# Optimization experiments

Hardware: AMD Instinct MI355X
Metric: run time of the kernel (lower is better)

## Reference

```python
import jax, jax.numpy as jnp
import numpy as np

DIM = 1028


def setup_inputs() -> dict:
    key = jax.random.key(0)
    ks = jax.random.split(key, 11)
    B, N = 8, 2048
    s = 0.02
    x = jax.random.normal(ks[0], (B, N, DIM), dtype=jnp.float32)
    Wq = jax.random.normal(ks[1], (DIM, DIM), dtype=jnp.float32) * s
    bq = jax.random.normal(ks[2], (DIM,), dtype=jnp.float32) * s
    Wk = jax.random.normal(ks[3], (DIM, DIM), dtype=jnp.float32) * s
    bk = jax.random.normal(ks[4], (DIM,), dtype=jnp.float32) * s
    Wv = jax.random.normal(ks[5], (DIM, DIM), dtype=jnp.float32) * s
    bv = jax.random.normal(ks[6], (DIM,), dtype=jnp.float32) * s
    We = jax.random.normal(ks[7], (4 * DIM, DIM), dtype=jnp.float32) * s
    be = jax.random.normal(ks[8], (4 * DIM,), dtype=jnp.float32) * s
    Wo = jax.random.normal(ks[9], (DIM, 4 * DIM), dtype=jnp.float32) * s
    bo = jax.random.normal(ks[10], (DIM,), dtype=jnp.float32) * s
    return {"x": x, "Wq": Wq, "bq": bq, "Wk": Wk, "bk": bk, "Wv": Wv,
            "bv": bv, "We": We, "be": be, "Wo": Wo, "bo": bo}


def reference(x, Wq, bq, Wk, bk, Wv, bv, We, be, Wo, bo):
    # x: [B, N, D]. torch Linear weight is [out, in] -> x @ W.T + b
    q = jnp.einsum('bnd,ed->bne', x, Wq) + bq
    k = jnp.einsum('bnd,ed->bne', x, Wk) + bk
    v = jnp.einsum('bnd,ed->bne', x, Wv) + bv
    scores = jnp.einsum('bqd,bkd->bqk', q, k) / jnp.sqrt(jnp.float32(DIM))
    w = jax.nn.softmax(scores, axis=-1)          # [B, N, N]
    attn = jnp.einsum('bqk,bkd->bqd', w, v)      # [B, N, D]
    h = jax.nn.gelu(jnp.einsum('bnd,hd->bnh', attn, We) + be, approximate=False)
    out = jnp.einsum('bnh,dh->bnd', h, Wo) + bo
    return out + x
```

## Files before the change

### kernel.cpp

```cpp
#include <hip/hip_runtime.h>
#include <hip/hip_bf16.h>
#include <cstdint>
#include <cmath>


typedef __bf16 bf16;
typedef __bf16 bf16x8 __attribute__((ext_vector_type(8)));
typedef float  f32x4  __attribute__((ext_vector_type(4)));

#define D_REAL   1028
#define D_PADK   1088
#define D_PADN   1152
#define H_REAL   4112
#define H_PAD    4224
#define NTOK     2048
#define NB       8
#define MTOT     (NB*NTOK)
#define SLAB_X   ((size_t)NTOK*D_PADK)
#define SLAB_S   ((size_t)NTOK*NTOK)
#define WSLAB    ((size_t)D_PADN*D_PADK)
#define VSLAB    ((size_t)D_PADN*NTOK)

__device__ __forceinline__ void async16(const void* g, void* l) {
    __builtin_amdgcn_global_load_lds(
        (__attribute__((address_space(1))) void*)(uintptr_t)g,
        (__attribute__((address_space(3))) void*)(uint32_t)(uintptr_t)l,
        16, 0, 0);
}

#define MFMA_(a, b, c) __builtin_amdgcn_mfma_f32_16x16x32_bf16(a, b, c, 0, 0, 0)

template <int EPI, bool XPIN>
__global__ __launch_bounds__(512, 2)
void gemm256(const bf16* __restrict__ A, size_t strideA,
             const bf16* __restrict__ B, size_t strideB,
             const float* __restrict__ bias, size_t strideBias,
             void* __restrict__ Out, size_t strideOut,
             bf16* __restrict__ OutV,
             int K, int outPitch, int colBound, float scale,
             const float* __restrict__ resid)
{
    __shared__ __attribute__((aligned(16))) bf16 sAB[4][256 * 64];

    int bx, by, bz;
    if (XPIN) {
        bz = blockIdx.x; by = blockIdx.y; bx = blockIdx.z;
    } else {
        const int nx   = gridDim.x;
        const int nwg  = nx * gridDim.y;
        const int orig = blockIdx.y * nx + blockIdx.x;
        const int q    = nwg >> 3;
        const int wg   = (orig & 7) * q + (orig >> 3);
        bx = wg % nx; by = wg / nx; bz = blockIdx.z;
    }

    A += (size_t)bz * strideA;
    B += (size_t)bz * strideB;
    if (bias) bias += (size_t)bz * strideBias;

    const int tid  = threadIdx.x;
    const int lane = tid & 63;
    const int wv   = tid >> 6;
    const int wm   = wv >> 2;
    const int wn   = wv & 3;

    const int    NT  = K >> 6;
    const size_t K64 = (size_t)K * 64;

    const int sRow = tid >> 3;
    const int sCh  = (tid & 7) ^ (sRow & 7);
    const bf16* gA = A + (size_t)(by * 256 + sRow) * K + sCh * 8;
    const bf16* gB = B + (size_t)(bx * 256 + sRow) * K + sCh * 8;
    const int ldsOff = sRow * 64 + (tid & 7) * 8;

#define STAGE_A(tt) do {                                           \
        const bf16* g_ = gA + (size_t)(tt) * 64;                   \
        bf16* l_ = &sAB[(tt) & 1][0] + ldsOff;                     \
        async16(g_,           l_);                                 \
        async16(g_ +     K64, l_ +  4096);                         \
        async16(g_ + 2 * K64, l_ +  8192);                         \
        async16(g_ + 3 * K64, l_ + 12288);                         \
    } while (0)
#define STAGE_B(tt) do {                                           \
        const bf16* g_ = gB + (size_t)(tt) * 64;                   \
        bf16* l_ = &sAB[2 + ((tt) & 1)][0] + ldsOff;               \
        async16(g_,           l_);                                 \
        async16(g_ +     K64, l_ +  4096);                         \
        async16(g_ + 2 * K64, l_ +  8192);                         \
        async16(g_ + 3 * K64, l_ + 12288);                         \
    } while (0)

    const int lr   = lane & 15;
    const int lq   = lane >> 4;
    const int rsw  = lr & 7;
    const int aRow = (wm * 128 + lr) * 64;
    const int bRow = (wn * 64  + lr) * 64;
    const int sl0  = (lq ^ rsw) << 3;
    const int sl1  = ((lq + 4) ^ rsw) << 3;

#define LDA_(i, s) (*(const bf16x8*)&sAc[aRow + (i) * 1024 + (s)])
#define LDB_(j, s) (*(const bf16x8*)&sBc[bRow + (j) * 1024 + (s)])

    f32x4 acc[8][4] = {};

    STAGE_A(0); STAGE_B(0);

    for (int t = 0; t < NT; ++t) {
        if (t + 1 < NT) {
            STAGE_A(t + 1);
            STAGE_B(t + 1);
            asm volatile("s_waitcnt vmcnt(8)" ::: "memory");
        } else {
            asm volatile("s_waitcnt vmcnt(0)" ::: "memory");
        }
        __builtin_amdgcn_s_barrier();
        __builtin_amdgcn_sched_barrier(0);

        const bf16* sAc = &sAB[t & 1][0];
        const bf16* sBc = &sAB[2 + (t & 1)][0];

        bf16x8 bfr[4][2];
        bfr[0][0] = LDB_(0, sl0); bfr[0][1] = LDB_(0, sl1);
        bfr[1][0] = LDB_(1, sl0); bfr[1][1] = LDB_(1, sl1);
        bfr[2][0] = LDB_(2, sl0); bfr[2][1] = LDB_(2, sl1);
        bfr[3][0] = LDB_(3, sl0); bfr[3][1] = LDB_(3, sl1);

        #pragma unroll
        for (int i = 0; i < 8; ++i) {
            const bf16x8 a0 = LDA_(i, sl0);
            const bf16x8 a1 = LDA_(i, sl1);
            acc[i][0] = MFMA_(a0, bfr[0][0], acc[i][0]);
            acc[i][1] = MFMA_(a0, bfr[1][0], acc[i][1]);
            acc[i][2] = MFMA_(a0, bfr[2][0], acc[i][2]);
            acc[i][3] = MFMA_(a0, bfr[3][0], acc[i][3]);
            acc[i][0] = MFMA_(a1, bfr[0][1], acc[i][0]);
            acc[i][1] = MFMA_(a1, bfr[1][1], acc[i][1]);
            acc[i][2] = MFMA_(a1, bfr[2][1], acc[i][2]);
            acc[i][3] = MFMA_(a1, bfr[3][1], acc[i][3]);
        }

        asm volatile("s_waitcnt lgkmcnt(0)" ::: "memory");
        __builtin_amdgcn_s_barrier();
        __builtin_amdgcn_sched_barrier(0);
    }

    #pragma unroll
    for (int i = 0; i < 8; ++i) {
        const int rowBase = by * 256 + wm * 128 + i * 16 + lq * 4;
        #pragma unroll
        for (int j = 0; j < 4; ++j) {
            f32x4 v = acc[i][j];
            const int cg = bx * 256 + wn * 64 + j * 16 + lr;
            if (cg >= colBound) continue;
            const float bs = bias ? bias[cg] : 0.0f;
            #pragma unroll
            for (int r = 0; r < 4; ++r) {
                const int mg = rowBase + r;
                const float val = v[r];
                if (EPI == 0) {
                    ((bf16*)Out + (size_t)bz * strideOut)[(size_t)mg * outPitch + cg] =
                        (bf16)(val + bs);
                } else if (EPI == 3) {
                    const float u = val + bs;
                    const float g = 0.5f * u * (1.0f + erff(u * 0.70710678118654752f));
                    ((bf16*)Out)[(size_t)mg * outPitch + cg] = (bf16)g;
                } else if (EPI == 4) {
                    ((float*)Out)[(size_t)mg * outPitch + cg] =
                        val + bs + resid[(size_t)mg * outPitch + cg];
                } else if (EPI == 5) {
                    const int grp = cg / D_PADN;
                    const int c   = cg - grp * D_PADN;
                    const float u = val + bs;
                    if (grp < 2) {
                        if (c < D_PADK)
                            ((bf16*)Out)[(size_t)bz * 2 * SLAB_X + (size_t)grp * SLAB_X +
                                         (size_t)mg * D_PADK + c] = (bf16)u;
                    } else {
                        OutV[(size_t)bz * VSLAB + (size_t)c * NTOK + mg] = (bf16)u;
                    }
                } else {
                    ((bf16*)Out + (size_t)bz * strideOut)[(size_t)mg * outPitch + cg] =
                        (bf16)(val * scale);
                }
            }
        }
    }
#undef STAGE_A
#undef STAGE_B
#undef LDA_
#undef LDB_
}

__global__ __launch_bounds__(256)
void cvt_pad(const float* __restrict__ src, int R, int C,
             bf16* __restrict__ dst, int CP)
{
    const int c = blockIdx.x * 256 + threadIdx.x;
    const int r = blockIdx.y;
    if (c >= CP) return;
    const float v = (r < R && c < C) ? src[(size_t)r * C + c] : 0.0f;
    dst[(size_t)r * CP + c] = (bf16)v;
}

__global__ __launch_bounds__(256)
void pad_bias(const float* __restrict__ src, int n, float* __restrict__ dst, int np)
{
    const int i = blockIdx.x * 256 + threadIdx.x;
    if (i < np) dst[i] = (i < n) ? src[i] : 0.0f;
}

__global__ __launch_bounds__(256)
void softmax_ip(bf16* __restrict__ S)
{
    const int row  = blockIdx.x * 4 + (threadIdx.x >> 6);
    const int lane = threadIdx.x & 63;
    bf16* s = S + (size_t)row * NTOK + lane * 8;

    float v[32];
    #pragma unroll
    for (int j = 0; j < 4; ++j) {
        bf16x8 t = *(const bf16x8*)(s + j * 512);
        #pragma unroll
        for (int e = 0; e < 8; ++e) v[j * 8 + e] = (float)t[e];
    }
    float m = -1e30f;
    #pragma unroll
    for (int i = 0; i < 32; ++i) m = fmaxf(m, v[i]);
    #pragma unroll
    for (int off = 32; off > 0; off >>= 1) m = fmaxf(m, __shfl_xor(m, off, 64));

    float sum = 0.0f;
    #pragma unroll
    for (int i = 0; i < 32; ++i) { v[i] = __expf(v[i] - m); sum += v[i]; }
    #pragma unroll
    for (int off = 32; off > 0; off >>= 1) sum += __shfl_xor(sum, off, 64);
    const float inv = 1.0f / sum;

    #pragma unroll
    for (int j = 0; j < 4; ++j) {
        bf16x8 t;
        #pragma unroll
        for (int e = 0; e < 8; ++e) t[e] = (bf16)(v[j * 8 + e] * inv);
        *(bf16x8*)(s + j * 512) = t;
    }
}

#define OFF_WQKV   0u
#define OFF_WE     7520256u
#define OFF_WO     16711680u
#define OFF_BQKV   26443776u
#define OFF_BE     26457600u
#define OFF_XBF    26474496u
#define OFF_VT     62126080u
#define OFF_SCR    99874816u
#define QS_BYTES   8912896u
#define SS_BYTES   8388608u

extern "C" void kernel_launch(void* const* d_in, const int* in_sizes, int n_in,
                              void* d_out, int out_size, void* d_ws, size_t ws_size,
                              hipStream_t stream)
{
    const float* x  = (const float*)d_in[0];
    const float* Wq = (const float*)d_in[1];
    const float* bq = (const float*)d_in[2];
    const float* Wk = (const float*)d_in[3];
    const float* bk = (const float*)d_in[4];
    const float* Wv = (const float*)d_in[5];
    const float* bv = (const float*)d_in[6];
    const float* We = (const float*)d_in[7];
    const float* be = (const float*)d_in[8];
    const float* Wo = (const float*)d_in[9];
    const float* bo = (const float*)d_in[10];

    char* ws = (char*)d_ws;
    bf16*  Wqkv = (bf16*)(ws + OFF_WQKV);
    bf16*  WeP  = (bf16*)(ws + OFF_WE);
    bf16*  WoP  = (bf16*)(ws + OFF_WO);
    float* Bqkv = (float*)(ws + OFF_BQKV);
    float* BeP  = (float*)(ws + OFF_BE);
    bf16*  Xbf  = (bf16*)(ws + OFF_XBF);
    bf16*  Vt   = (bf16*)(ws + OFF_VT);
    char*  scr  = ws + OFF_SCR;

    const size_t avail = ws_size > OFF_SCR ? ws_size - OFF_SCR : 0;
    const size_t perG  = (size_t)QS_BYTES + SS_BYTES;
    int G = (avail >= 8 * perG) ? 8 : (avail >= 4 * perG) ? 4
          : (avail >= 2 * perG) ? 2 : 1;
    int R = (avail >= 69206016u) ? 8192 : (avail >= 34603008u) ? 4096 : 2048;

    bf16* Qs = (bf16*)scr;
    bf16* Ss = (bf16*)(scr + (size_t)G * QS_BYTES);
    bf16* Hb = (bf16*)scr;

    const dim3 blk(256);
    const dim3 blkG(512);
    const float inv_sqrt_d = (float)(1.0 / sqrt((double)D_REAL));

    cvt_pad<<<dim3(5, MTOT), blk, 0, stream>>>(x, MTOT, D_REAL, Xbf, D_PADK);
    cvt_pad<<<dim3(5, D_PADN), blk, 0, stream>>>(Wq, D_REAL, D_REAL, Wqkv, D_PADK);
    cvt_pad<<<dim3(5, D_PADN), blk, 0, stream>>>(Wk, D_REAL, D_REAL, Wqkv + WSLAB, D_PADK);
    cvt_pad<<<dim3(5, D_PADN), blk, 0, stream>>>(Wv, D_REAL, D_REAL, Wqkv + 2 * WSLAB, D_PADK);
    cvt_pad<<<dim3(5, H_PAD), blk, 0, stream>>>(We, H_REAL, D_REAL, WeP, D_PADK);
    cvt_pad<<<dim3(17, D_PADN), blk, 0, stream>>>(Wo, D_REAL, H_REAL, WoP, H_PAD);
    pad_bias<<<dim3(5), blk, 0, stream>>>(bq, D_REAL, Bqkv, D_PADN);
    pad_bias<<<dim3(5), blk, 0, stream>>>(bk, D_REAL, Bqkv + D_PADN, D_PADN);
    pad_bias<<<dim3(5), blk, 0, stream>>>(bv, D_REAL, Bqkv + 2 * D_PADN, D_PADN);
    pad_bias<<<dim3(17), blk, 0, stream>>>(be, H_REAL, BeP, H_PAD);

    for (int g0 = 0; g0 < NB; g0 += G) {
        gemm256<5, false><<<dim3(14, 8, G), blkG, 0, stream>>>(
            Xbf + (size_t)g0 * SLAB_X, SLAB_X, Wqkv, 0, Bqkv, 0,
            Qs, 0, Vt + (size_t)g0 * VSLAB,
            D_PADK, 0, 3456, 1.0f, nullptr);
        gemm256<6, true><<<dim3(G, 8, 8), blkG, 0, stream>>>(
            Qs, 2 * SLAB_X, Qs + SLAB_X, 2 * SLAB_X, nullptr, 0,
            Ss, SLAB_S, nullptr, D_PADK, NTOK, NTOK, inv_sqrt_d, nullptr);
        softmax_ip<<<dim3(G * 512), blk, 0, stream>>>(Ss);
        gemm256<0, true><<<dim3(G, 8, 5), blkG, 0, stream>>>(
            Ss, SLAB_S, Vt + (size_t)g0 * VSLAB, VSLAB, nullptr, 0,
            Xbf + (size_t)g0 * SLAB_X, SLAB_X, nullptr,
            NTOK, D_PADK, D_PADK, 1.0f, nullptr);
    }

    for (int r0 = 0; r0 < MTOT; r0 += R) {
        gemm256<3, false><<<dim3(17, R / 256, 1), blkG, 0, stream>>>(
            Xbf + (size_t)r0 * D_PADK, 0, WeP, 0, BeP, 0,
            Hb, 0, nullptr, D_PADK, H_PAD, H_PAD, 1.0f, nullptr);
        gemm256<4, false><<<dim3(5, R / 256, 1), blkG, 0, stream>>>(
            Hb, 0, WoP, 0, bo, 0,
            (float*)d_out + (size_t)r0 * D_REAL, 0, nullptr,
            H_PAD, D_REAL, D_REAL, 1.0f, x + (size_t)r0 * D_REAL);
    }
}
```

Baseline: 1.136 ms.

## Interleave split global-to-LDS staging with MFMA phases in GEMM main loop

The bf16 GEMM main loop is split into four compute phases of two row blocks each. The A and B tile loads are broken into halves and issued between these phases: A for the next tile, and B two tiles ahead, since the B fragments are already held in registers. The goal is to overlap global-to-LDS transfers with MFMA work instead of issuing them all at the top of each iteration. The compute sections also raise wave priority with s_setprio. In exchange, the loop needs many more barriers and hand-tuned vmcnt/lgkmcnt waits, and any mistake in that counting risks read-after-write races on the two LDS buffers.

Result: slower. 1.164 ms (+2.5%).

```diff
diff --git a/kernel.cpp b/kernel.cpp
--- a/kernel.cpp
+++ b/kernel.cpp
@@ -73,21 +73,17 @@
     const bf16* gB = B + (size_t)(bx * 256 + sRow) * K + sCh * 8;
     const int ldsOff = sRow * 64 + (tid & 7) * 8;
 
-#define STAGE_A(tt) do {                                           \
-        const bf16* g_ = gA + (size_t)(tt) * 64;                   \
-        bf16* l_ = &sAB[(tt) & 1][0] + ldsOff;                     \
-        async16(g_,           l_);                                 \
-        async16(g_ +     K64, l_ +  4096);                         \
-        async16(g_ + 2 * K64, l_ +  8192);                         \
-        async16(g_ + 3 * K64, l_ + 12288);                         \
+#define STAGE_A_HALF(tt, h) do {                                        \
+        const bf16* g_ = gA + (size_t)(tt) * 64 + (size_t)(2*(h)) * K64;\
+        bf16* l_ = &sAB[(tt) & 1][0] + ldsOff + (2*(h)) * 4096;         \
+        async16(g_,       l_);                                          \
+        async16(g_ + K64, l_ + 4096);                                   \
     } while (0)
-#define STAGE_B(tt) do {                                           \
-        const bf16* g_ = gB + (size_t)(tt) * 64;                   \
-        bf16* l_ = &sAB[2 + ((tt) & 1)][0] + ldsOff;               \
-        async16(g_,           l_);                                 \
-        async16(g_ +     K64, l_ +  4096);                         \
-        async16(g_ + 2 * K64, l_ +  8192);                         \
-        async16(g_ + 3 * K64, l_ + 12288);                         \
+#define STAGE_B_HALF(tt, h) do {                                        \
+        const bf16* g_ = gB + (size_t)(tt) * 64 + (size_t)(2*(h)) * K64;\
+        bf16* l_ = &sAB[2 + ((tt) & 1)][0] + ldsOff + (2*(h)) * 4096;   \
+        async16(g_,       l_);                                          \
+        async16(g_ + K64, l_ + 4096);                                   \
     } while (0)
 
     const int lr   = lane & 15;
@@ -103,45 +99,76 @@
 
     f32x4 acc[8][4] = {};
 
-    STAGE_A(0); STAGE_B(0);
+#define MM(i, x0, x1) do {                                  \
+        acc[i][0] = MFMA_(x0, bfr[0][0], acc[i][0]);        \
+        acc[i][1] = MFMA_(x0, bfr[1][0], acc[i][1]);        \
+        acc[i][2] = MFMA_(x0, bfr[2][0], acc[i][2]);        \
+        acc[i][3] = MFMA_(x0, bfr[3][0], acc[i][3]);        \
+        acc[i][0] = MFMA_(x1, bfr[0][1], acc[i][0]);        \
+        acc[i][1] = MFMA_(x1, bfr[1][1], acc[i][1]);        \
+        acc[i][2] = MFMA_(x1, bfr[2][1], acc[i][2]);        \
+        acc[i][3] = MFMA_(x1, bfr[3][1], acc[i][3]);        \
+    } while (0)
+
+    STAGE_A_HALF(0, 0); STAGE_A_HALF(0, 1);
+    STAGE_B_HALF(0, 0); STAGE_B_HALF(0, 1);
+    STAGE_A_HALF(1, 0); STAGE_A_HALF(1, 1);
+    STAGE_B_HALF(1, 0); STAGE_B_HALF(1, 1);
+    asm volatile("s_waitcnt vmcnt(8)" ::: "memory");
+    __builtin_amdgcn_s_barrier();
 
     for (int t = 0; t < NT; ++t) {
-        if (t + 1 < NT) {
-            STAGE_A(t + 1);
-            STAGE_B(t + 1);
-            asm volatile("s_waitcnt vmcnt(8)" ::: "memory");
-        } else {
-            asm volatile("s_waitcnt vmcnt(0)" ::: "memory");
-        }
-        __builtin_amdgcn_s_barrier();
-        __builtin_amdgcn_sched_barrier(0);
-
         const bf16* sAc = &sAB[t & 1][0];
         const bf16* sBc = &sAB[2 + (t & 1)][0];
-
         bf16x8 bfr[4][2];
+        bf16x8 x0, x1, x2, x3;
+
         bfr[0][0] = LDB_(0, sl0); bfr[0][1] = LDB_(0, sl1);
         bfr[1][0] = LDB_(1, sl0); bfr[1][1] = LDB_(1, sl1);
         bfr[2][0] = LDB_(2, sl0); bfr[2][1] = LDB_(2, sl1);
         bfr[3][0] = LDB_(3, sl0); bfr[3][1] = LDB_(3, sl1);
-
-        #pragma unroll
-        for (int i = 0; i < 8; ++i) {
-            const bf16x8 a0 = LDA_(i, sl0);
-            const bf16x8 a1 = LDA_(i, sl1);
-            acc[i][0] = MFMA_(a0, bfr[0][0], acc[i][0]);
-            acc[i][1] = MFMA_(a0, bfr[1][0], acc[i][1]);
-            acc[i][2] = MFMA_(a0, bfr[2][0], acc[i][2]);
-            acc[i][3] = MFMA_(a0, bfr[3][0], acc[i][3]);
-            acc[i][0] = MFMA_(a1, bfr[0][1], acc[i][0]);
-            acc[i][1] = MFMA_(a1, bfr[1][1], acc[i][1]);
-            acc[i][2] = MFMA_(a1, bfr[2][1], acc[i][2]);
-            acc[i][3] = MFMA_(a1, bfr[3][1], acc[i][3]);
-        }
-
+        x0 = LDA_(0, sl0); x1 = LDA_(0, sl1);
+        x2 = LDA_(1, sl0); x3 = LDA_(1, sl1);
+        if (t > 0 && t + 1 < NT) STAGE_A_HALF(t + 1, 0);
+        asm volatile("s_waitcnt lgkmcnt(8)" ::: "memory");
+        __builtin_amdgcn_s_barrier();
         asm volatile("s_waitcnt lgkmcnt(0)" ::: "memory");
-        __builtin_amdgcn_s_barrier();
-        __builtin_amdgcn_sched_barrier(0);
+        __builtin_amdgcn_s_setprio(1);
+        MM(0, x0, x1); MM(1, x2, x3);
+        __builtin_amdgcn_s_setprio(0);
+        __builtin_amdgcn_s_barrier();
+
+        x0 = LDA_(2, sl0); x1 = LDA_(2, sl1);
+        x2 = LDA_(3, sl0); x3 = LDA_(3, sl1);
+        if (t > 0 && t + 1 < NT) STAGE_A_HALF(t + 1, 1);
+        __builtin_amdgcn_s_barrier();
+        asm volatile("s_waitcnt lgkmcnt(0)" ::: "memory");
+        __builtin_amdgcn_s_setprio(1);
+        MM(2, x0, x1); MM(3, x2, x3);
+        __builtin_amdgcn_s_setprio(0);
+        __builtin_amdgcn_s_barrier();
+
+        x0 = LDA_(4, sl0); x1 = LDA_(4, sl1);
+        x2 = LDA_(5, sl0); x3 = LDA_(5, sl1);
+        if (t + 2 < NT) STAGE_B_HALF(t + 2, 0);
+        __builtin_amdgcn_s_barrier();
+        asm volatile("s_waitcnt lgkmcnt(0)" ::: "memory");
+        __builtin_amdgcn_s_setprio(1);
+        MM(4, x0, x1); MM(5, x2, x3);
+        __builtin_amdgcn_s_setprio(0);
+        __builtin_amdgcn_s_barrier();
+
+        x0 = LDA_(6, sl0); x1 = LDA_(6, sl1);
+        x2 = LDA_(7, sl0); x3 = LDA_(7, sl1);
+        if (t + 2 < NT) STAGE_B_HALF(t + 2, 1);
+        __builtin_amdgcn_s_barrier();
+        asm volatile("s_waitcnt lgkmcnt(0)" ::: "memory");
+        __builtin_amdgcn_s_setprio(1);
+        MM(6, x0, x1); MM(7, x2, x3);
+        __builtin_amdgcn_s_setprio(0);
+        if (t + 2 < NT)       asm volatile("s_waitcnt vmcnt(4)" ::: "memory");
+        else if (t + 1 < NT)  asm volatile("s_waitcnt vmcnt(0)" ::: "memory");
+        __builtin_amdgcn_s_barrier();
     }
 
     #pragma unroll
@@ -185,10 +212,11 @@
             }
         }
     }
-#undef STAGE_A
-#undef STAGE_B
+#undef STAGE_A_HALF
+#undef STAGE_B_HALF
 #undef LDA_
 #undef LDB_
+#undef MM
 }
 
 __global__ __launch_bounds__(256)
```
